# Optimization experiments

Hardware: AMD Instinct MI355X
Metric: run time of the kernel (lower is better)

Reference implementation:

```python
import jax, jax.numpy as jnp
import numpy as np

# Dimensions: B jets, P max particles, C coords, F features, K neighbors,
# H hidden units, O MLP output dim. Edge feature dim E = 2*(C+F).
B, P, C, F, K, H, O = 256, 128, 2, 7, 16, 128, 256
E = 2 * (C + F)
BIG = 1e9  # distance assigned to invalid (padded) neighbors


def setup_inputs() -> dict:
    key = jax.random.key(0)
    k1, k2, k3, k4 = jax.random.split(key, 4)
    raw = jax.random.normal(k1, (B, P, C + F), dtype=jnp.float32)
    # per-jet particle counts in [K+2, P]; padding is contiguous at the end
    lengths = jax.random.randint(k2, (B,), K + 2, P + 1)
    mask = (jnp.arange(P)[None, :] < lengths[:, None]).astype(jnp.float32)  # [B,P]
    # zero out padded rows and append mask as the last column (as the layer expects)
    x = jnp.concatenate([raw * mask[..., None], mask[..., None]], axis=-1)  # [B,P,C+F+1]
    W1 = jax.random.normal(k3, (E, H), dtype=jnp.float32) * (1.0 / np.sqrt(E))
    b1 = jnp.zeros((H,), dtype=jnp.float32)
    W2 = jax.random.normal(k4, (H, O), dtype=jnp.float32) * (1.0 / np.sqrt(H))
    b2 = jnp.zeros((O,), dtype=jnp.float32)
    return {"x": x, "W1": W1, "b1": b1, "W2": W2, "b2": b2}


def reference(x, W1, b1, W2, b2):
    coords = x[..., :C]          # [B,P,C]
    feats = x[..., C:-1]         # [B,P,F]
    mask = x[..., -1]            # [B,P] 1=real particle, 0=padding
    valid = mask > 0

    # --- kNN on coordinates (masked, vectorized over jets) ---
    diff = coords[:, :, None, :] - coords[:, None, :, :]      # [B,P,P,C]
    # squared distance: same ordering as tf.norm, avoids sqrt-at-zero issues
    dist2 = jnp.sum(diff * diff, axis=-1)                      # [B,P,P]
    dist2 = jnp.where(valid[:, None, :], dist2, BIG)           # mask padded neighbors
    _, idx = jax.lax.top_k(-dist2, K + 1)                      # [B,P,K+1]
    idx = idx[..., 1:]                                         # drop self -> [B,P,K]

    # --- gather neighbor coords/features ---
    idx_flat = idx.reshape(B, P * K)
    nbr_c = jnp.take_along_axis(coords, idx_flat[..., None], axis=1).reshape(B, P, K, C)
    nbr_f = jnp.take_along_axis(feats, idx_flat[..., None], axis=1).reshape(B, P, K, F)
    ctr_c = jnp.broadcast_to(coords[:, :, None, :], (B, P, K, C))
    ctr_f = jnp.broadcast_to(feats[:, :, None, :], (B, P, K, F))

    # edge features: [coord_i, feat_i, coord_j - coord_i, feat_j - feat_i]
    edge = jnp.concatenate([ctr_c, ctr_f, nbr_c - ctr_c, nbr_f - ctr_f], axis=-1)  # [B,P,K,E]

    # --- MLP + mean aggregation over neighbors ---
    h = jax.nn.relu(edge @ W1 + b1)   # [B,P,K,H]
    h = jax.nn.relu(h @ W2 + b2)      # [B,P,K,O]
    avg = jnp.mean(h, axis=2)         # [B,P,O]

    # append mask column; zero out padded particles (matches _fix_number_of_particles)
    out = jnp.concatenate([avg, jnp.ones((B, P, 1), avg.dtype)], axis=-1) * mask[..., None]
    return out
```

## Files before the change

### kernel.cpp

```cpp
#include <hip/hip_runtime.h>

#define BB 256
#define PP 128
#define KK 16
#define HH 128
#define OO 256
#define EE 18
#define XCH 10
#define BIGD 1000000000.0f
#define GPT 8
#define NBLK ((BB * PP) / GPT)

typedef __bf16 bf16x8 __attribute__((ext_vector_type(8)));
typedef __bf16 bf16x4 __attribute__((ext_vector_type(4)));
typedef float  f32x4  __attribute__((ext_vector_type(4)));

__global__ __launch_bounds__(256) void pack_w_kernel(const float* __restrict__ W1,
                                                     const float* __restrict__ W2,
                                                     __bf16* __restrict__ W2p,
                                                     __bf16* __restrict__ W1p) {
    const int t = blockIdx.x * 256 + threadIdx.x;
    if (t < 32768) {
        const int j  = t & 7;
        const int l  = (t >> 3) & 63;
        const int ks = (t >> 9) & 3;
        const int ct = t >> 11;
        const int row = ks * 32 + ((l >> 4) * 8) + j;
        const int col = ct * 16 + (l & 15);
        W2p[t] = (__bf16)W2[row * OO + col];
    } else {
        const int t2 = t - 32768;
        const int j  = t2 & 7;
        const int l  = (t2 >> 3) & 63;
        const int nt = t2 >> 9;
        const int k  = ((l >> 4) * 8) + j;
        const int n  = nt * 16 + (l & 15);
        W1p[t2] = (k < EE) ? (__bf16)W1[k * HH + n] : (__bf16)0.0f;
    }
}

__global__ __launch_bounds__(512, 4) void mlp_kernel(const float* __restrict__ x,
                                                     const __bf16* __restrict__ W1p,
                                                     const float* __restrict__ b1,
                                                     const __bf16* __restrict__ W2p,
                                                     const float* __restrict__ b2,
                                                     float* __restrict__ out) {
    __shared__ __bf16 sh1A[32 * 64 * 8];
    __shared__ int    sknn[GPT][KK];

    const int tid = threadIdx.x;
    const int lane = tid & 63;
    const int w = tid >> 6;
    const int quad = lane >> 4;
    const int lcol = lane & 15;

    const int pbase = blockIdx.x * GPT;
    const int bidx = pbase >> 7;
    const int i0 = pbase & (PP - 1);
    const float* xb = x + (size_t)bidx * PP * XCH;
    float* outrow = out + (size_t)pbase * (OO + 1);

    const float m_lo = xb[(i0 + quad) * XCH + (XCH - 1)];
    const float m_hi = xb[(i0 + 4 + quad) * XCH + (XCH - 1)];
    const int i = i0 + w;

    if (__all((m_lo == 0.0f) & (m_hi == 0.0f))) {
        for (int o = tid; o < GPT * (OO + 1); o += 512) outrow[o] = 0.0f;
        return;
    }

    bf16x8 wf[8];
#pragma unroll
    for (int nt = 0; nt < 8; ++nt)
        wf[nt] = *(const bf16x8*)&W1p[(size_t)((nt * 64 + lane) * 8)];

    const float* ci = xb + i * XCH;
    const float2 a01 = *(const float2*)(ci + 0);
    const float2 a23 = *(const float2*)(ci + 2);
    const float2 a45 = *(const float2*)(ci + 4);
    const float2 a67 = *(const float2*)(ci + 6);
    const float  a8  = ci[8];
    const float  mw  = ci[XCH - 1];

    if (mw != 0.0f) {
        const float cix = a01.x;
        const float ciy = a01.y;

        const int j0 = lane, j1 = lane + 64;
        float d0, d1;
        {
            const float2 c0 = *(const float2*)(xb + j0 * XCH);
            const float m0 = xb[j0 * XCH + (XCH - 1)];
            float dx = cix - c0.x, dy = ciy - c0.y;
            d0 = __fadd_rn(__fmul_rn(dx, dx), __fmul_rn(dy, dy));
            if (m0 <= 0.0f || j0 == i) d0 = BIGD;
        }
        {
            const float2 c1 = *(const float2*)(xb + j1 * XCH);
            const float m1 = xb[j1 * XCH + (XCH - 1)];
            float dx = cix - c1.x, dy = ciy - c1.y;
            d1 = __fadd_rn(__fmul_rn(dx, dx), __fmul_rn(dy, dy));
            if (m1 <= 0.0f || j1 == i) d1 = BIGD;
        }

        const unsigned d0b = __float_as_uint(d0);
        const unsigned d1b = __float_as_uint(d1);

        unsigned long long A0 = ~0ull, A1 = ~0ull, W0 = 0ull, W1 = 0ull;
        int need = KK;
        int asz = 2 * 64;

        auto step = [&](unsigned long long q0, unsigned long long q1) {
            const unsigned long long z0 = A0 & q0;
            const unsigned long long z1 = A1 & q1;
            const int c = __popcll(z0) + __popcll(z1);
            if (c == need) { W0 |= z0; W1 |= z1; A0 = A1 = 0ull; need = 0; }
            else if (c > need) { A0 = z0; A1 = z1; asz = c; }
            else { W0 |= z0; W1 |= z1; need -= c; A0 &= ~z0; A1 &= ~z1; asz -= c; }
        };

#pragma unroll 1
        for (int t = 14; t >= 0; --t) {
            const unsigned dg0 = (d0b >> (2 * t + 1)) & 3u;
            const unsigned dg1 = (d1b >> (2 * t + 1)) & 3u;
            const unsigned long long p0_0  = __ballot(dg0 == 0u);
            const unsigned long long p1_0  = __ballot(dg1 == 0u);
            const unsigned long long p0_01 = __ballot(dg0 <= 1u);
            const unsigned long long p1_01 = __ballot(dg1 <= 1u);
            const unsigned long long p0_02 = __ballot(dg0 <= 2u);
            const unsigned long long p1_02 = __ballot(dg1 <= 2u);
            const unsigned long long z0_0  = A0 & p0_0,  z1_0  = A1 & p1_0;
            const unsigned long long z0_01 = A0 & p0_01, z1_01 = A1 & p1_01;
            const unsigned long long z0_02 = A0 & p0_02, z1_02 = A1 & p1_02;
            const int c0  = __popcll(z0_0)  + __popcll(z1_0);
            const int c01 = __popcll(z0_01) + __popcll(z1_01);
            const int c02 = __popcll(z0_02) + __popcll(z1_02);
            if (c0 >= need) {
                A0 = z0_0; A1 = z1_0; asz = c0;
            } else if (c01 >= need) {
                W0 |= z0_0; W1 |= z1_0; need -= c0;
                A0 = z0_01 & ~p0_0; A1 = z1_01 & ~p1_0; asz = c01 - c0;
            } else if (c02 >= need) {
                W0 |= z0_01; W1 |= z1_01; need -= c01;
                A0 = z0_02 & ~p0_01; A1 = z1_02 & ~p1_01; asz = c02 - c01;
            } else {
                W0 |= z0_02; W1 |= z1_02; need -= c02;
                A0 &= ~p0_02; A1 &= ~p1_02; asz -= c02;
            }
            if (asz == need) { W0 |= A0; W1 |= A1; A0 = A1 = 0ull; need = 0; break; }
        }
        if (need) {
            const unsigned long long q0 = __ballot((d0b & 1u) == 0u);
            const unsigned long long q1 = __ballot((d1b & 1u) == 0u);
            step(q0, q1);
        }
        if (need) step(~0ull, 0ull);
        {
            const unsigned long long M5 = 0x00000000FFFFFFFFull;
            const unsigned long long M4 = 0x0000FFFF0000FFFFull;
            const unsigned long long M3 = 0x00FF00FF00FF00FFull;
            const unsigned long long M2 = 0x0F0F0F0F0F0F0F0Full;
            const unsigned long long M1 = 0x3333333333333333ull;
            const unsigned long long M0 = 0x5555555555555555ull;
            if (need) step(M5, M5);
            if (need) step(M4, M4);
            if (need) step(M3, M3);
            if (need) step(M2, M2);
            if (need) step(M1, M1);
            if (need) step(M0, M0);
        }
        W0 |= A0; W1 |= A1;

        unsigned int mb0 = __builtin_amdgcn_mbcnt_lo((unsigned)(W0 & 0xffffffffull), 0u);
        mb0 = __builtin_amdgcn_mbcnt_hi((unsigned)(W0 >> 32), mb0);
        unsigned int mb1 = __builtin_amdgcn_mbcnt_lo((unsigned)(W1 & 0xffffffffull), 0u);
        mb1 = __builtin_amdgcn_mbcnt_hi((unsigned)(W1 >> 32), mb1);
        const int base1 = __popcll(W0);

        if ((W0 >> lane) & 1ull) sknn[w][mb0] = j0;
        if ((W1 >> lane) & 1ull) sknn[w][base1 + mb1] = j1;
    } else {
        if (lane < KK) sknn[w][lane] = 0;
    }

    const int jn = sknn[w][lcol];
    const float* cj = xb + jn * XCH;
    const float2 n01 = *(const float2*)(cj + 0);
    const float2 n23 = *(const float2*)(cj + 2);
    const float2 n45 = *(const float2*)(cj + 4);
    const float2 n67 = *(const float2*)(cj + 6);
    const float  n8  = cj[8];

    float v[8];
#pragma unroll
    for (int e = 0; e < 8; ++e) v[e] = 0.0f;
    if (quad == 0) {
        v[0] = a01.x; v[1] = a01.y; v[2] = a23.x; v[3] = a23.y;
        v[4] = a45.x; v[5] = a45.y; v[6] = a67.x; v[7] = a67.y;
    } else if (quad == 1) {
        v[0] = a8;
        v[1] = n01.x - a01.x; v[2] = n01.y - a01.y;
        v[3] = n23.x - a23.x; v[4] = n23.y - a23.y;
        v[5] = n45.x - a45.x; v[6] = n45.y - a45.y;
        v[7] = n67.x - a67.x;
    } else if (quad == 2) {
        v[0] = n67.y - a67.y;
        v[1] = n8 - a8;
    }

    bf16x8 ef;
#pragma unroll
    for (int e = 0; e < 8; ++e) ef[e] = (__bf16)v[e];

    const f32x4 z4 = {0.0f, 0.0f, 0.0f, 0.0f};
    f32x4 h[8];
#pragma unroll
    for (int nt = 0; nt < 8; ++nt)
        h[nt] = __builtin_amdgcn_mfma_f32_16x16x32_bf16(wf[nt], ef, z4, 0, 0, 0);

#pragma unroll
    for (int nt = 0; nt < 8; ++nt) {
        const int ks = nt >> 1;
        const int lp = (((nt * 2 + (quad >> 1)) & 3) << 4) | lcol;
        const f32x4 b1v = *(const f32x4*)&b1[nt * 16 + quad * 4];
        bf16x4 hv;
#pragma unroll
        for (int r = 0; r < 4; ++r)
            hv[r] = (__bf16)fmaxf(h[nt][r] + b1v[r], 0.0f);
        *(bf16x4*)&sh1A[((ks * GPT + w) * 64 + lp) * 8 + (quad & 1) * 4] = hv;
    }
    __syncthreads();

#pragma unroll
    for (int gh = 0; gh < 2; ++gh) {
        f32x4 acc[4][2];
#pragma unroll
        for (int gi = 0; gi < 4; ++gi) { acc[gi][0] = z4; acc[gi][1] = z4; }

#pragma unroll
        for (int ks = 0; ks < 4; ++ks) {
            bf16x8 af[4], bfr[2];
#pragma unroll
            for (int gi = 0; gi < 4; ++gi)
                af[gi] = *(const bf16x8*)&sh1A[((ks * GPT + gh * 4 + gi) * 64 + lane) * 8];
#pragma unroll
            for (int c = 0; c < 2; ++c)
                bfr[c] = *(const bf16x8*)&W2p[(size_t)((((w * 2 + c) * 4 + ks) * 64 + lane) * 8)];
#pragma unroll
            for (int gi = 0; gi < 4; ++gi)
#pragma unroll
                for (int c = 0; c < 2; ++c)
                    acc[gi][c] = __builtin_amdgcn_mfma_f32_16x16x32_bf16(
                        af[gi], bfr[c], acc[gi][c], 0, 0, 0);
        }

        const float mp = (gh == 0) ? m_lo : m_hi;
        const float mscale = mp * (1.0f / KK);
#pragma unroll
        for (int c = 0; c < 2; ++c) {
            const int col = w * 32 + c * 16 + lcol;
            const float bc = b2[col];
            float val = 0.0f;
#pragma unroll
            for (int gi = 0; gi < 4; ++gi) {
                float s = 0.0f;
#pragma unroll
                for (int r = 0; r < 4; ++r) s += fmaxf(acc[gi][c][r] + bc, 0.0f);
                s += __shfl_xor(s, 16, 64);
                s += __shfl_xor(s, 32, 64);
                if (quad == gi) val = s;
            }
            outrow[(size_t)(gh * 4 + quad) * (OO + 1) + col] = val * mscale;
        }
    }
    if (tid < GPT) outrow[(size_t)tid * (OO + 1) + OO] = xb[(i0 + tid) * XCH + (XCH - 1)];
}

extern "C" void kernel_launch(void* const* d_in, const int* in_sizes, int n_in,
                              void* d_out, int out_size, void* d_ws, size_t ws_size,
                              hipStream_t stream) {
    const float* x  = (const float*)d_in[0];
    const float* W1 = (const float*)d_in[1];
    const float* b1 = (const float*)d_in[2];
    const float* W2 = (const float*)d_in[3];
    const float* b2 = (const float*)d_in[4];
    float* out = (float*)d_out;

    __bf16* W2p = (__bf16*)d_ws;
    __bf16* W1p = (__bf16*)((char*)d_ws + 65536);

    pack_w_kernel<<<144, 256, 0, stream>>>(W1, W2, W2p, W1p);

    mlp_kernel<<<NBLK, 512, 0, stream>>>(x, W1p, b1, W2p, b2, out);
}
```

Measured before the change: 134.7 us.

## Process 16 particles per 4-wave block in two halves with reused weights

Blocks shrink from 8 waves to 4 waves but now cover 16 particles, split into two halves of 8. Each wave runs kNN and the first MLP layer for two particles per half. In the second layer each wave computes 64 output columns instead of 32, and the all-padding early-out is checked per half. The aim is to load W1 fragments and neighbor coordinates once per more particles, raise per-wave work and halve block count. The cost is serialised per-wave kNN work and an extra barrier per half.

```diff
diff --git a/kernel.cpp b/kernel.cpp
--- a/kernel.cpp
+++ b/kernel.cpp
@@ -8,7 +8,8 @@
 #define EE 18
 #define XCH 10
 #define BIGD 1000000000.0f
-#define GPT 8
+#define GPT 16
+#define PH 8
 #define NBLK ((BB * PP) / GPT)
 
 typedef __bf16 bf16x8 __attribute__((ext_vector_type(8)));
@@ -39,14 +40,14 @@
     }
 }
 
-__global__ __launch_bounds__(512, 4) void mlp_kernel(const float* __restrict__ x,
+__global__ __launch_bounds__(256, 4) void mlp_kernel(const float* __restrict__ x,
                                                      const __bf16* __restrict__ W1p,
                                                      const float* __restrict__ b1,
                                                      const __bf16* __restrict__ W2p,
                                                      const float* __restrict__ b2,
                                                      float* __restrict__ out) {
-    __shared__ __bf16 sh1A[32 * 64 * 8];
-    __shared__ int    sknn[GPT][KK];
+    __shared__ __bf16 sh1A[4 * PH * 64 * 8];
+    __shared__ int    sknn[PH][KK];
 
     const int tid = threadIdx.x;
     const int lane = tid & 63;
@@ -60,220 +61,237 @@
     const float* xb = x + (size_t)bidx * PP * XCH;
     float* outrow = out + (size_t)pbase * (OO + 1);
 
-    const float m_lo = xb[(i0 + quad) * XCH + (XCH - 1)];
-    const float m_hi = xb[(i0 + 4 + quad) * XCH + (XCH - 1)];
-    const int i = i0 + w;
-
-    if (__all((m_lo == 0.0f) & (m_hi == 0.0f))) {
-        for (int o = tid; o < GPT * (OO + 1); o += 512) outrow[o] = 0.0f;
-        return;
-    }
-
     bf16x8 wf[8];
 #pragma unroll
     for (int nt = 0; nt < 8; ++nt)
         wf[nt] = *(const bf16x8*)&W1p[(size_t)((nt * 64 + lane) * 8)];
 
-    const float* ci = xb + i * XCH;
-    const float2 a01 = *(const float2*)(ci + 0);
-    const float2 a23 = *(const float2*)(ci + 2);
-    const float2 a45 = *(const float2*)(ci + 4);
-    const float2 a67 = *(const float2*)(ci + 6);
-    const float  a8  = ci[8];
-    const float  mw  = ci[XCH - 1];
-
-    if (mw != 0.0f) {
-        const float cix = a01.x;
-        const float ciy = a01.y;
+    const f32x4 z4 = {0.0f, 0.0f, 0.0f, 0.0f};
+
+#pragma unroll
+    for (int h = 0; h < 2; ++h) {
+        const int r0 = h * PH;
+
+        const float mph = xb[(i0 + r0 + (lane & 7)) * XCH + (XCH - 1)];
+        if (__all(mph == 0.0f)) {
+            for (int o = tid; o < PH * (OO + 1); o += 256)
+                outrow[(size_t)r0 * (OO + 1) + o] = 0.0f;
+            continue;
+        }
 
         const int j0 = lane, j1 = lane + 64;
-        float d0, d1;
-        {
-            const float2 c0 = *(const float2*)(xb + j0 * XCH);
-            const float m0 = xb[j0 * XCH + (XCH - 1)];
-            float dx = cix - c0.x, dy = ciy - c0.y;
-            d0 = __fadd_rn(__fmul_rn(dx, dx), __fmul_rn(dy, dy));
-            if (m0 <= 0.0f || j0 == i) d0 = BIGD;
+        const float2 c0 = *(const float2*)(xb + j0 * XCH);
+        const float  m0 = xb[j0 * XCH + (XCH - 1)];
+        const float2 c1 = *(const float2*)(xb + j1 * XCH);
+        const float  m1 = xb[j1 * XCH + (XCH - 1)];
+
+#pragma unroll 1
+        for (int p = 0; p < 2; ++p) {
+            const int g = w * 2 + p;
+            const int ip = i0 + r0 + g;
+            const float2 cc = *(const float2*)(xb + ip * XCH);
+            const float mwp = xb[ip * XCH + (XCH - 1)];
+            if (mwp != 0.0f) {
+                float d0, d1;
+                {
+                    float dx = cc.x - c0.x, dy = cc.y - c0.y;
+                    d0 = __fadd_rn(__fmul_rn(dx, dx), __fmul_rn(dy, dy));
+                    if (m0 <= 0.0f || j0 == ip) d0 = BIGD;
+                }
+                {
+                    float dx = cc.x - c1.x, dy = cc.y - c1.y;
+                    d1 = __fadd_rn(__fmul_rn(dx, dx), __fmul_rn(dy, dy));
+                    if (m1 <= 0.0f || j1 == ip) d1 = BIGD;
+                }
+
+                const unsigned d0b = __float_as_uint(d0);
+                const unsigned d1b = __float_as_uint(d1);
+
+                unsigned long long A0 = ~0ull, A1 = ~0ull, W0 = 0ull, W1 = 0ull;
+                int need = KK;
+                int asz = 2 * 64;
+
+                auto step = [&](unsigned long long q0, unsigned long long q1) {
+                    const unsigned long long z0 = A0 & q0;
+                    const unsigned long long z1 = A1 & q1;
+                    const int c = __popcll(z0) + __popcll(z1);
+                    if (c == need) { W0 |= z0; W1 |= z1; A0 = A1 = 0ull; need = 0; }
+                    else if (c > need) { A0 = z0; A1 = z1; asz = c; }
+                    else { W0 |= z0; W1 |= z1; need -= c; A0 &= ~z0; A1 &= ~z1; asz -= c; }
+                };
+
+#pragma unroll 1
+                for (int t = 14; t >= 0; --t) {
+                    const unsigned dg0 = (d0b >> (2 * t + 1)) & 3u;
+                    const unsigned dg1 = (d1b >> (2 * t + 1)) & 3u;
+                    const unsigned long long p0_0  = __ballot(dg0 == 0u);
+                    const unsigned long long p1_0  = __ballot(dg1 == 0u);
+                    const unsigned long long p0_01 = __ballot(dg0 <= 1u);
+                    const unsigned long long p1_01 = __ballot(dg1 <= 1u);
+                    const unsigned long long p0_02 = __ballot(dg0 <= 2u);
+                    const unsigned long long p1_02 = __ballot(dg1 <= 2u);
+                    const unsigned long long z0_0  = A0 & p0_0,  z1_0  = A1 & p1_0;
+                    const unsigned long long z0_01 = A0 & p0_01, z1_01 = A1 & p1_01;
+                    const unsigned long long z0_02 = A0 & p0_02, z1_02 = A1 & p1_02;
+                    const int c0c  = __popcll(z0_0)  + __popcll(z1_0);
+                    const int c01 = __popcll(z0_01) + __popcll(z1_01);
+                    const int c02 = __popcll(z0_02) + __popcll(z1_02);
+                    if (c0c >= need) {
+                        A0 = z0_0; A1 = z1_0; asz = c0c;
+                    } else if (c01 >= need) {
+                        W0 |= z0_0; W1 |= z1_0; need -= c0c;
+                        A0 = z0_01 & ~p0_0; A1 = z1_01 & ~p1_0; asz = c01 - c0c;
+                    } else if (c02 >= need) {
+                        W0 |= z0_01; W1 |= z1_01; need -= c01;
+                        A0 = z0_02 & ~p0_01; A1 = z1_02 & ~p1_01; asz = c02 - c01;
+                    } else {
+                        W0 |= z0_02; W1 |= z1_02; need -= c02;
+                        A0 &= ~p0_02; A1 &= ~p1_02; asz -= c02;
+                    }
+                    if (asz == need) { W0 |= A0; W1 |= A1; A0 = A1 = 0ull; need = 0; break; }
+                }
+                if (need) {
+                    const unsigned long long q0 = __ballot((d0b & 1u) == 0u);
+                    const unsigned long long q1 = __ballot((d1b & 1u) == 0u);
+                    step(q0, q1);
+                }
+                if (need) step(~0ull, 0ull);
+                {
+                    const unsigned long long M5 = 0x00000000FFFFFFFFull;
+                    const unsigned long long M4 = 0x0000FFFF0000FFFFull;
+                    const unsigned long long M3 = 0x00FF00FF00FF00FFull;
+                    const unsigned long long M2 = 0x0F0F0F0F0F0F0F0Full;
+                    const unsigned long long M1 = 0x3333333333333333ull;
+                    const unsigned long long M0 = 0x5555555555555555ull;
+                    if (need) step(M5, M5);
+                    if (need) step(M4, M4);
+                    if (need) step(M3, M3);
+                    if (need) step(M2, M2);
+                    if (need) step(M1, M1);
+                    if (need) step(M0, M0);
+                }
+                W0 |= A0; W1 |= A1;
+
+                unsigned int mb0 = __builtin_amdgcn_mbcnt_lo((unsigned)(W0 & 0xffffffffull), 0u);
+                mb0 = __builtin_amdgcn_mbcnt_hi((unsigned)(W0 >> 32), mb0);
+                unsigned int mb1 = __builtin_amdgcn_mbcnt_lo((unsigned)(W1 & 0xffffffffull), 0u);
+                mb1 = __builtin_amdgcn_mbcnt_hi((unsigned)(W1 >> 32), mb1);
+                const int base1 = __popcll(W0);
+
+                if ((W0 >> lane) & 1ull) sknn[g][mb0] = j0;
+                if ((W1 >> lane) & 1ull) sknn[g][base1 + mb1] = j1;
+            } else {
+                if (lane < KK) sknn[g][lane] = 0;
+            }
         }
-        {
-            const float2 c1 = *(const float2*)(xb + j1 * XCH);
-            const float m1 = xb[j1 * XCH + (XCH - 1)];
-            float dx = cix - c1.x, dy = ciy - c1.y;
-            d1 = __fadd_rn(__fmul_rn(dx, dx), __fmul_rn(dy, dy));
-            if (m1 <= 0.0f || j1 == i) d1 = BIGD;
+
+#pragma unroll
+        for (int p = 0; p < 2; ++p) {
+            const int g = w * 2 + p;
+            const int ip = i0 + r0 + g;
+            const int jn = sknn[g][lcol];
+            const float* ciP = xb + ip * XCH;
+            const float* cjP = xb + jn * XCH;
+            const float2 a01 = *(const float2*)(ciP + 0);
+            const float2 a23 = *(const float2*)(ciP + 2);
+            const float2 a45 = *(const float2*)(ciP + 4);
+            const float2 a67 = *(const float2*)(ciP + 6);
+            const float  a8  = ciP[8];
+            const float2 n01 = *(const float2*)(cjP + 0);
+            const float2 n23 = *(const float2*)(cjP + 2);
+            const float2 n45 = *(const float2*)(cjP + 4);
+            const float2 n67 = *(const float2*)(cjP + 6);
+            const float  n8  = cjP[8];
+
+            float v[8];
+#pragma unroll
+            for (int e = 0; e < 8; ++e) v[e] = 0.0f;
+            if (quad == 0) {
+                v[0] = a01.x; v[1] = a01.y; v[2] = a23.x; v[3] = a23.y;
+                v[4] = a45.x; v[5] = a45.y; v[6] = a67.x; v[7] = a67.y;
+            } else if (quad == 1) {
+                v[0] = a8;
+                v[1] = n01.x - a01.x; v[2] = n01.y - a01.y;
+                v[3] = n23.x - a23.x; v[4] = n23.y - a23.y;
+                v[5] = n45.x - a45.x; v[6] = n45.y - a45.y;
+                v[7] = n67.x - a67.x;
+            } else if (quad == 2) {
+                v[0] = n67.y - a67.y;
+                v[1] = n8 - a8;
+            }
+
+            bf16x8 ef;
+#pragma unroll
+            for (int e = 0; e < 8; ++e) ef[e] = (__bf16)v[e];
+
+            f32x4 hh[8];
+#pragma unroll
+            for (int nt = 0; nt < 8; ++nt)
+                hh[nt] = __builtin_amdgcn_mfma_f32_16x16x32_bf16(wf[nt], ef, z4, 0, 0, 0);
+
+#pragma unroll
+            for (int nt = 0; nt < 8; ++nt) {
+                const int ks = nt >> 1;
+                const int lp = (((nt * 2 + (quad >> 1)) & 3) << 4) | lcol;
+                const f32x4 b1v = *(const f32x4*)&b1[nt * 16 + quad * 4];
+                bf16x4 hv;
+#pragma unroll
+                for (int r = 0; r < 4; ++r)
+                    hv[r] = (__bf16)fmaxf(hh[nt][r] + b1v[r], 0.0f);
+                *(bf16x4*)&sh1A[((ks * PH + g) * 64 + lp) * 8 + (quad & 1) * 4] = hv;
+            }
         }
-
-        const unsigned d0b = __float_as_uint(d0);
-        const unsigned d1b = __float_as_uint(d1);
-
-        unsigned long long A0 = ~0ull, A1 = ~0ull, W0 = 0ull, W1 = 0ull;
-        int need = KK;
-        int asz = 2 * 64;
-
-        auto step = [&](unsigned long long q0, unsigned long long q1) {
-            const unsigned long long z0 = A0 & q0;
-            const unsigned long long z1 = A1 & q1;
-            const int c = __popcll(z0) + __popcll(z1);
-            if (c == need) { W0 |= z0; W1 |= z1; A0 = A1 = 0ull; need = 0; }
-            else if (c > need) { A0 = z0; A1 = z1; asz = c; }
-            else { W0 |= z0; W1 |= z1; need -= c; A0 &= ~z0; A1 &= ~z1; asz -= c; }
-        };
-
-#pragma unroll 1
-        for (int t = 14; t >= 0; --t) {
-            const unsigned dg0 = (d0b >> (2 * t + 1)) & 3u;
-            const unsigned dg1 = (d1b >> (2 * t + 1)) & 3u;
-            const unsigned long long p0_0  = __ballot(dg0 == 0u);
-            const unsigned long long p1_0  = __ballot(dg1 == 0u);
-            const unsigned long long p0_01 = __ballot(dg0 <= 1u);
-            const unsigned long long p1_01 = __ballot(dg1 <= 1u);
-            const unsigned long long p0_02 = __ballot(dg0 <= 2u);
-            const unsigned long long p1_02 = __ballot(dg1 <= 2u);
-            const unsigned long long z0_0  = A0 & p0_0,  z1_0  = A1 & p1_0;
-            const unsigned long long z0_01 = A0 & p0_01, z1_01 = A1 & p1_01;
-            const unsigned long long z0_02 = A0 & p0_02, z1_02 = A1 & p1_02;
-            const int c0  = __popcll(z0_0)  + __popcll(z1_0);
-            const int c01 = __popcll(z0_01) + __popcll(z1_01);
-            const int c02 = __popcll(z0_02) + __popcll(z1_02);
-            if (c0 >= need) {
-                A0 = z0_0; A1 = z1_0; asz = c0;
-            } else if (c01 >= need) {
-                W0 |= z0_0; W1 |= z1_0; need -= c0;
-                A0 = z0_01 & ~p0_0; A1 = z1_01 & ~p1_0; asz = c01 - c0;
-            } else if (c02 >= need) {
-                W0 |= z0_01; W1 |= z1_01; need -= c01;
-                A0 = z0_02 & ~p0_01; A1 = z1_02 & ~p1_01; asz = c02 - c01;
-            } else {
-                W0 |= z0_02; W1 |= z1_02; need -= c02;
-                A0 &= ~p0_02; A1 &= ~p1_02; asz -= c02;
+        __syncthreads();
+
+#pragma unroll
+        for (int gg = 0; gg < 2; ++gg) {
+#pragma unroll
+            for (int ch = 0; ch < 2; ++ch) {
+                f32x4 acc[4][2];
+#pragma unroll
+                for (int gi = 0; gi < 4; ++gi) { acc[gi][0] = z4; acc[gi][1] = z4; }
+
+#pragma unroll
+                for (int ks = 0; ks < 4; ++ks) {
+                    bf16x8 af[4], bfr[2];
+#pragma unroll
+                    for (int gi = 0; gi < 4; ++gi)
+                        af[gi] = *(const bf16x8*)&sh1A[((ks * PH + gg * 4 + gi) * 64 + lane) * 8];
+#pragma unroll
+                    for (int c = 0; c < 2; ++c)
+                        bfr[c] = *(const bf16x8*)&W2p[(size_t)((((w * 4 + ch * 2 + c) * 4 + ks) * 64 + lane) * 8)];
+#pragma unroll
+                    for (int gi = 0; gi < 4; ++gi)
+#pragma unroll
+                        for (int c = 0; c < 2; ++c)
+                            acc[gi][c] = __builtin_amdgcn_mfma_f32_16x16x32_bf16(
+                                af[gi], bfr[c], acc[gi][c], 0, 0, 0);
+                }
+
+#pragma unroll
+                for (int c = 0; c < 2; ++c) {
+                    const int col = w * 64 + (ch * 2 + c) * 16 + lcol;
+                    const float bc = b2[col];
+                    float val = 0.0f;
+#pragma unroll
+                    for (int gi = 0; gi < 4; ++gi) {
+                        float s = 0.0f;
+#pragma unroll
+                        for (int r = 0; r < 4; ++r) s += fmaxf(acc[gi][c][r] + bc, 0.0f);
+                        s += __shfl_xor(s, 16, 64);
+                        s += __shfl_xor(s, 32, 64);
+                        if (quad == gi) val = s;
+                    }
+                    const float mp = xb[(i0 + r0 + gg * 4 + quad) * XCH + (XCH - 1)];
+                    outrow[(size_t)(r0 + gg * 4 + quad) * (OO + 1) + col] = val * (mp * (1.0f / KK));
+                }
             }
-            if (asz == need) { W0 |= A0; W1 |= A1; A0 = A1 = 0ull; need = 0; break; }
         }
-        if (need) {
-            const unsigned long long q0 = __ballot((d0b & 1u) == 0u);
-            const unsigned long long q1 = __ballot((d1b & 1u) == 0u);
-            step(q0, q1);
-        }
-        if (need) step(~0ull, 0ull);
-        {
-            const unsigned long long M5 = 0x00000000FFFFFFFFull;
-            const unsigned long long M4 = 0x0000FFFF0000FFFFull;
-            const unsigned long long M3 = 0x00FF00FF00FF00FFull;
-            const unsigned long long M2 = 0x0F0F0F0F0F0F0F0Full;
-            const unsigned long long M1 = 0x3333333333333333ull;
-            const unsigned long long M0 = 0x5555555555555555ull;
-            if (need) step(M5, M5);
-            if (need) step(M4, M4);
-            if (need) step(M3, M3);
-            if (need) step(M2, M2);
-            if (need) step(M1, M1);
-            if (need) step(M0, M0);
-        }
-        W0 |= A0; W1 |= A1;
-
-        unsigned int mb0 = __builtin_amdgcn_mbcnt_lo((unsigned)(W0 & 0xffffffffull), 0u);
-        mb0 = __builtin_amdgcn_mbcnt_hi((unsigned)(W0 >> 32), mb0);
-        unsigned int mb1 = __builtin_amdgcn_mbcnt_lo((unsigned)(W1 & 0xffffffffull), 0u);
-        mb1 = __builtin_amdgcn_mbcnt_hi((unsigned)(W1 >> 32), mb1);
-        const int base1 = __popcll(W0);
-
-        if ((W0 >> lane) & 1ull) sknn[w][mb0] = j0;
-        if ((W1 >> lane) & 1ull) sknn[w][base1 + mb1] = j1;
-    } else {
-        if (lane < KK) sknn[w][lane] = 0;
+        if (tid < PH)
+            outrow[(size_t)(r0 + tid) * (OO + 1) + OO] = xb[(i0 + r0 + tid) * XCH + (XCH - 1)];
+
+        __syncthreads();
     }
-
-    const int jn = sknn[w][lcol];
-    const float* cj = xb + jn * XCH;
-    const float2 n01 = *(const float2*)(cj + 0);
-    const float2 n23 = *(const float2*)(cj + 2);
-    const float2 n45 = *(const float2*)(cj + 4);
-    const float2 n67 = *(const float2*)(cj + 6);
-    const float  n8  = cj[8];
-
-    float v[8];
-#pragma unroll
-    for (int e = 0; e < 8; ++e) v[e] = 0.0f;
-    if (quad == 0) {
-        v[0] = a01.x; v[1] = a01.y; v[2] = a23.x; v[3] = a23.y;
-        v[4] = a45.x; v[5] = a45.y; v[6] = a67.x; v[7] = a67.y;
-    } else if (quad == 1) {
-        v[0] = a8;
-        v[1] = n01.x - a01.x; v[2] = n01.y - a01.y;
-        v[3] = n23.x - a23.x; v[4] = n23.y - a23.y;
-        v[5] = n45.x - a45.x; v[6] = n45.y - a45.y;
-        v[7] = n67.x - a67.x;
-    } else if (quad == 2) {
-        v[0] = n67.y - a67.y;
-        v[1] = n8 - a8;
-    }
-
-    bf16x8 ef;
-#pragma unroll
-    for (int e = 0; e < 8; ++e) ef[e] = (__bf16)v[e];
-
-    const f32x4 z4 = {0.0f, 0.0f, 0.0f, 0.0f};
-    f32x4 h[8];
-#pragma unroll
-    for (int nt = 0; nt < 8; ++nt)
-        h[nt] = __builtin_amdgcn_mfma_f32_16x16x32_bf16(wf[nt], ef, z4, 0, 0, 0);
-
-#pragma unroll
-    for (int nt = 0; nt < 8; ++nt) {
-        const int ks = nt >> 1;
-        const int lp = (((nt * 2 + (quad >> 1)) & 3) << 4) | lcol;
-        const f32x4 b1v = *(const f32x4*)&b1[nt * 16 + quad * 4];
-        bf16x4 hv;
-#pragma unroll
-        for (int r = 0; r < 4; ++r)
-            hv[r] = (__bf16)fmaxf(h[nt][r] + b1v[r], 0.0f);
-        *(bf16x4*)&sh1A[((ks * GPT + w) * 64 + lp) * 8 + (quad & 1) * 4] = hv;
-    }
-    __syncthreads();
-
-#pragma unroll
-    for (int gh = 0; gh < 2; ++gh) {
-        f32x4 acc[4][2];
-#pragma unroll
-        for (int gi = 0; gi < 4; ++gi) { acc[gi][0] = z4; acc[gi][1] = z4; }
-
-#pragma unroll
-        for (int ks = 0; ks < 4; ++ks) {
-            bf16x8 af[4], bfr[2];
-#pragma unroll
-            for (int gi = 0; gi < 4; ++gi)
-                af[gi] = *(const bf16x8*)&sh1A[((ks * GPT + gh * 4 + gi) * 64 + lane) * 8];
-#pragma unroll
-            for (int c = 0; c < 2; ++c)
-                bfr[c] = *(const bf16x8*)&W2p[(size_t)((((w * 2 + c) * 4 + ks) * 64 + lane) * 8)];
-#pragma unroll
-            for (int gi = 0; gi < 4; ++gi)
-#pragma unroll
-                for (int c = 0; c < 2; ++c)
-                    acc[gi][c] = __builtin_amdgcn_mfma_f32_16x16x32_bf16(
-                        af[gi], bfr[c], acc[gi][c], 0, 0, 0);
-        }
-
-        const float mp = (gh == 0) ? m_lo : m_hi;
-        const float mscale = mp * (1.0f / KK);
-#pragma unroll
-        for (int c = 0; c < 2; ++c) {
-            const int col = w * 32 + c * 16 + lcol;
-            const float bc = b2[col];
-            float val = 0.0f;
-#pragma unroll
-            for (int gi = 0; gi < 4; ++gi) {
-                float s = 0.0f;
-#pragma unroll
-                for (int r = 0; r < 4; ++r) s += fmaxf(acc[gi][c][r] + bc, 0.0f);
-                s += __shfl_xor(s, 16, 64);
-                s += __shfl_xor(s, 32, 64);
-                if (quad == gi) val = s;
-            }
-            outrow[(size_t)(gh * 4 + quad) * (OO + 1) + col] = val * mscale;
-        }
-    }
-    if (tid < GPT) outrow[(size_t)tid * (OO + 1) + OO] = xb[(i0 + tid) * XCH + (XCH - 1)];
 }
 
 extern "C" void kernel_launch(void* const* d_in, const int* in_sizes, int n_in,
@@ -291,5 +309,5 @@
 
     pack_w_kernel<<<144, 256, 0, stream>>>(W1, W2, W2p, W1p);
 
-    mlp_kernel<<<NBLK, 512, 0, stream>>>(x, W1p, b1, W2p, b2, out);
+    mlp_kernel<<<NBLK, 256, 0, stream>>>(x, W1p, b1, W2p, b2, out);
 }
```

Result: no change. 133.1 us (-1.2%).
